# Kernel tuning notes

Measured on AMD Instinct MI355X. Metric: run time of the kernel, lower is better.

Reference implementation:

```python
import jax, jax.numpy as jnp
import numpy as np

N = 50000      # nodes
E = 800000     # edges (before self loops)
G = 64         # graphs in batch
IN = 128       # in_features
HID = 64       # hidden_dim per head
HEADS = 4
NC = 2         # num_classes
SLOPE = 0.2    # PyG GATConv negative_slope default


def setup_inputs() -> dict:
    key = jax.random.key(0)
    ks = jax.random.split(key, 16)
    s = 0.1
    HC = HID * HEADS
    inp = {
        "x": jax.random.normal(ks[0], (N, IN), jnp.float32),
        "edge_index": jax.random.randint(ks[1], (2, E), 0, N, jnp.int64),
        "batch": jnp.sort(jax.random.randint(ks[2], (N,), 0, G, jnp.int64)),
        # GATConv 1: lin weight [H*C, IN], att vecs [H, C], bias [H*C]
        "W1": jax.random.normal(ks[3], (HC, IN), jnp.float32) * s,
        "as1": jax.random.normal(ks[4], (HEADS, HID), jnp.float32) * s,
        "ad1": jax.random.normal(ks[5], (HEADS, HID), jnp.float32) * s,
        "b1": jnp.zeros((HC,), jnp.float32),
        # GATConv 2
        "W2": jax.random.normal(ks[6], (HC, HC), jnp.float32) * s,
        "as2": jax.random.normal(ks[7], (HEADS, HID), jnp.float32) * s,
        "ad2": jax.random.normal(ks[8], (HEADS, HID), jnp.float32) * s,
        "b2": jnp.zeros((HC,), jnp.float32),
        # GATConv 3
        "W3": jax.random.normal(ks[9], (HC, HC), jnp.float32) * s,
        "as3": jax.random.normal(ks[10], (HEADS, HID), jnp.float32) * s,
        "ad3": jax.random.normal(ks[11], (HEADS, HID), jnp.float32) * s,
        "b3": jnp.zeros((HC,), jnp.float32),
        # MLP head
        "fc1_w": jax.random.normal(ks[12], (HID, HC), jnp.float32) * s,
        "fc1_b": jnp.zeros((HID,), jnp.float32),
        "fc2_w": jax.random.normal(ks[13], (NC, HID), jnp.float32) * s,
        "fc2_b": jnp.zeros((NC,), jnp.float32),
    }
    return inp


def gat_conv(x, src, dst, W, a_src, a_dst, b):
    """PyG-style GATConv (concat=True, self loops already in src/dst)."""
    n = x.shape[0]
    h = (x @ W.T).reshape(n, HEADS, HID)            # [N,H,C]
    al_s = jnp.sum(h * a_src[None], axis=-1)        # [N,H]
    al_d = jnp.sum(h * a_dst[None], axis=-1)        # [N,H]
    e = jax.nn.leaky_relu(al_s[src] + al_d[dst], SLOPE)  # [Et,H]
    # segment softmax over edges grouped by destination node
    m = jax.ops.segment_max(e, dst, num_segments=n)      # [N,H]
    ex = jnp.exp(e - m[dst])
    den = jax.ops.segment_sum(ex, dst, num_segments=n)
    alpha = ex / (den[dst] + 1e-16)                      # [Et,H]
    out = jax.ops.segment_sum(h[src] * alpha[:, :, None], dst, num_segments=n)
    return out.reshape(n, HEADS * HID) + b


def reference(x, edge_index, batch, W1, as1, ad1, b1, W2, as2, ad2, b2,
              W3, as3, ad3, b3, fc1_w, fc1_b, fc2_w, fc2_b):
    loops = jnp.arange(N, dtype=edge_index.dtype)
    src = jnp.concatenate([edge_index[0], loops])   # add_self_loops=True
    dst = jnp.concatenate([edge_index[1], loops])

    h = jax.nn.relu(gat_conv(x, src, dst, W1, as1, ad1, b1))
    h = jax.nn.relu(gat_conv(h, src, dst, W2, as2, ad2, b2))
    h = gat_conv(h, src, dst, W3, as3, ad3, b3)

    # global_mean_pool over batch vector
    sums = jax.ops.segment_sum(h, batch, num_segments=G)          # [G,H*C]
    cnts = jax.ops.segment_sum(jnp.ones((N,), h.dtype), batch, num_segments=G)
    pooled = sums / jnp.maximum(cnts, 1.0)[:, None]

    z = jax.nn.relu(pooled @ fc1_w.T + fc1_b)
    return z @ fc2_w.T + fc2_b                                    # [G,NC]
```

## Files before the change

### kernel.cpp

```cpp
#include <hip/hip_runtime.h>
#include <hip/hip_bf16.h>

#define N_NODES 50000
#define E_EDGES 800000
#define ET (E_EDGES + N_NODES)
#define G_GRAPHS 64
#define IN_F 128
#define HID 64
#define HEADS 4
#define HC (HID * HEADS)
#define NC 2
#define SLOPE 0.2f
#define L2E 1.4426950408889634f

typedef float f32x4 __attribute__((ext_vector_type(4)));
typedef __bf16 bf16x8 __attribute__((ext_vector_type(8)));
typedef unsigned short us8 __attribute__((ext_vector_type(8)));
typedef unsigned short us4 __attribute__((ext_vector_type(4)));
typedef _Float16 h16x4 __attribute__((ext_vector_type(4)));

#define MFMA16(a, b, c) \
  __builtin_amdgcn_mfma_f32_16x16x32_bf16(__builtin_bit_cast(bf16x8, (a)), \
                                          __builtin_bit_cast(bf16x8, (b)), (c), 0, 0, 0)

__device__ inline unsigned short f2bf_rne(float f) {
  unsigned u = __builtin_bit_cast(unsigned, f);
  u += 0x7fffu + ((u >> 16) & 1u);
  return (unsigned short)(u >> 16);
}
__device__ inline float bf2f(unsigned short h) {
  unsigned u = ((unsigned)h) << 16;
  return __builtin_bit_cast(float, u);
}


__device__ inline void split4(const float* __restrict__ in, unsigned short* __restrict__ hi,
                              unsigned short* __restrict__ lo, int i) {
  float4 v = *(const float4*)&in[i];
  float f[4] = {v.x, v.y, v.z, v.w};
  us4 h, l;
#pragma unroll
  for (int j = 0; j < 4; j++) {
    unsigned short hb = f2bf_rne(f[j]);
    h[j] = hb;
    l[j] = f2bf_rne(f[j] - bf2f(hb));
  }
  *(us4*)&hi[i] = h;
  *(us4*)&lo[i] = l;
}

#define QX (N_NODES * IN_F / 4)
#define QW1 (HC * IN_F / 4)
#define QW2 (HC * HC / 4)
#define QTOT (QX + QW1 + 2 * QW2)

__global__ __launch_bounds__(256) void split_all_kernel(
    const float* __restrict__ x, const float* __restrict__ W1,
    const float* __restrict__ W2, const float* __restrict__ W3,
    unsigned short* __restrict__ xhi,
    unsigned short* __restrict__ w1h, unsigned short* __restrict__ w1l,
    unsigned short* __restrict__ w2h, unsigned short* __restrict__ w2l,
    unsigned short* __restrict__ w3h, unsigned short* __restrict__ w3l) {
  int q = blockIdx.x * 256 + threadIdx.x;
  if (q < QX) {
    int i = q * 4;
    float4 v = *(const float4*)&x[i];
    float f[4] = {v.x, v.y, v.z, v.w};
    us4 h;
#pragma unroll
    for (int j = 0; j < 4; j++) h[j] = f2bf_rne(f[j]);
    *(us4*)&xhi[i] = h;
  } else if (q < QX + QW1) {
    split4(W1, w1h, w1l, (q - QX) * 4);
  } else if (q < QX + QW1 + QW2) {
    split4(W2, w2h, w2l, (q - QX - QW1) * 4);
  } else {
    split4(W3, w3h, w3l, (q - QX - QW1 - QW2) * 4);
  }
}


__global__ void count_kernel(const int* __restrict__ ei, int* __restrict__ cnt) {
  int e = blockIdx.x * blockDim.x + threadIdx.x;
  if (e >= ET) return;
  int dst = (e < E_EDGES) ? ei[E_EDGES + e] : (e - E_EDGES);
  atomicAdd(&cnt[dst], 1);
}

#define SCAN_BLOCKS ((N_NODES + 255) / 256)

__global__ __launch_bounds__(256) void scan1_kernel(const int* __restrict__ cnt,
                                                    int* __restrict__ incl_buf,
                                                    int* __restrict__ partial) {
  __shared__ int ws[4];
  int tid = threadIdx.x, b = blockIdx.x;
  int wave = tid >> 6, lane = tid & 63;
  int i = b * 256 + tid;
  int v = (i < N_NODES) ? cnt[i] : 0;
  int x = v;
#pragma unroll
  for (int off = 1; off < 64; off <<= 1) {
    int t = __shfl_up(x, off, 64);
    if (lane >= off) x += t;
  }
  if (lane == 63) ws[wave] = x;
  __syncthreads();
  if (tid == 0) {
    int s = 0;
#pragma unroll
    for (int w = 0; w < 4; w++) { int t = ws[w]; ws[w] = s; s += t; }
    partial[b] = s;
  }
  __syncthreads();
  if (i < N_NODES) incl_buf[i] = x + ws[wave];
}

__global__ __launch_bounds__(256) void scan2_kernel(int* __restrict__ partial) {
  __shared__ int ws[4];
  int tid = threadIdx.x;
  int wave = tid >> 6, lane = tid & 63;
  int v = (tid < SCAN_BLOCKS) ? partial[tid] : 0;
  int x = v;
#pragma unroll
  for (int off = 1; off < 64; off <<= 1) {
    int t = __shfl_up(x, off, 64);
    if (lane >= off) x += t;
  }
  if (lane == 63) ws[wave] = x;
  __syncthreads();
  if (tid == 0) {
    int s = 0;
#pragma unroll
    for (int w = 0; w < 4; w++) { int t = ws[w]; ws[w] = s; s += t; }
  }
  __syncthreads();
  partial[tid] = x + ws[wave] - v;
}

__global__ __launch_bounds__(256) void scan3_kernel(const int* __restrict__ cnt,
                                                    int* __restrict__ incl_buf,
                                                    const int* __restrict__ partial,
                                                    int* __restrict__ rowptr,
                                                    int* __restrict__ cursor) {
  int tid = threadIdx.x, b = blockIdx.x;
  int i = b * 256 + tid;
  if (i >= N_NODES) return;
  int incl = incl_buf[i] + partial[b];
  rowptr[i + 1] = incl;
  cursor[i] = incl - cnt[i];
  if (i == 0) rowptr[0] = 0;
}

__global__ void scatter_kernel(const int* __restrict__ ei, int* __restrict__ cursor,
                               int* __restrict__ csr_src) {
  int e = blockIdx.x * blockDim.x + threadIdx.x;
  if (e >= ET) return;
  int src, dst;
  if (e < E_EDGES) { src = ei[e]; dst = ei[E_EDGES + e]; }
  else { src = e - E_EDGES; dst = src; }
  int pos = atomicAdd(&cursor[dst], 1);
  csr_src[pos] = src;
}


template <int K>
__global__ __launch_bounds__(256) void mfma_gemm_kernel(
    const unsigned short* __restrict__ A,
    const unsigned short* __restrict__ Whi, const unsigned short* __restrict__ Wlo,
    const float* __restrict__ a_s, const float* __restrict__ a_d,
    _Float16* __restrict__ hbuf16, float* __restrict__ als, float* __restrict__ ald) {
  __shared__ unsigned short As[4 * 64 * 8];
  __shared__ unsigned short Bs[2][4 * 256 * 8];

  int t = threadIdx.x;
  int mt = blockIdx.x;
  int w = t >> 6, lane = t & 63, lr = lane & 15, kg = lane >> 4;
  int srow = t >> 2, skg = t & 3;

  f32x4 acc[4][4];
#pragma unroll
  for (int m = 0; m < 4; m++)
#pragma unroll
    for (int nf = 0; nf < 4; nf++) {
      f32x4 z = {0.f, 0.f, 0.f, 0.f};
      acc[m][nf] = z;
    }

  int agrow = mt * 64 + srow;
  bool avalid = agrow < N_NODES;

  for (int k0 = 0; k0 < K; k0 += 32) {
    us8 va;
    if (avalid) {
      va = *(const us8*)&A[(size_t)agrow * K + k0 + skg * 8];
    } else {
      us8 z = {0, 0, 0, 0, 0, 0, 0, 0};
      va = z;
    }
    us8 vb0[4], vb1[4];
#pragma unroll
    for (int c = 0; c < 4; c++) {
      int n = srow + 64 * c;
      vb0[c] = *(const us8*)&Whi[(size_t)n * K + k0 + skg * 8];
      vb1[c] = *(const us8*)&Wlo[(size_t)n * K + k0 + skg * 8];
    }
    __syncthreads();
    *(us8*)&As[(skg * 64 + srow) * 8] = va;
#pragma unroll
    for (int c = 0; c < 4; c++) {
      int n = srow + 64 * c;
      *(us8*)&Bs[0][(skg * 256 + n) * 8] = vb0[c];
      *(us8*)&Bs[1][(skg * 256 + n) * 8] = vb1[c];
    }
    __syncthreads();

    us8 bh[4], bl[4];
#pragma unroll
    for (int nf = 0; nf < 4; nf++) {
      int n = w * 64 + nf * 16 + lr;
      bh[nf] = *(us8*)&Bs[0][(kg * 256 + n) * 8];
      bl[nf] = *(us8*)&Bs[1][(kg * 256 + n) * 8];
    }
#pragma unroll
    for (int m = 0; m < 4; m++) {
      int row = m * 16 + lr;
      us8 ah = *(us8*)&As[(kg * 64 + row) * 8];
#pragma unroll
      for (int nf = 0; nf < 4; nf++) {
        acc[m][nf] = MFMA16(ah, bh[nf], acc[m][nf]);
        acc[m][nf] = MFMA16(ah, bl[nf], acc[m][nf]);
      }
    }
  }

  int head = w;
  float asv[4], adv[4];
#pragma unroll
  for (int nf = 0; nf < 4; nf++) {
    asv[nf] = a_s[head * HID + nf * 16 + lr];
    adv[nf] = a_d[head * HID + nf * 16 + lr];
  }
#pragma unroll
  for (int m = 0; m < 4; m++) {
#pragma unroll
    for (int r = 0; r < 4; r++) {
      int grow = mt * 64 + m * 16 + kg * 4 + r;
      float ps = 0.f, pd = 0.f;
#pragma unroll
      for (int nf = 0; nf < 4; nf++) {
        float v = acc[m][nf][r];
        ps += v * asv[nf];
        pd += v * adv[nf];
        if (grow < N_NODES)
          hbuf16[(size_t)grow * HC + head * 64 + nf * 16 + lr] = (_Float16)v;
      }
#pragma unroll
      for (int msk = 1; msk < 16; msk <<= 1) {
        ps += __shfl_xor(ps, msk, 64);
        pd += __shfl_xor(pd, msk, 64);
      }
      if (lr == 0 && grow < N_NODES) {
        als[grow * HEADS + head] = ps * L2E;
        ald[grow * HEADS + head] = pd * L2E;
      }
    }
  }
}


template <int MODE>
__global__ __launch_bounds__(256) void agg_kernel(
    const _Float16* __restrict__ hbuf16, const float* __restrict__ alsE,
    const float* __restrict__ aldE, const int* __restrict__ rowptr,
    const int* __restrict__ csr_src, const float* __restrict__ bias,
    unsigned short* __restrict__ ohi, float* __restrict__ pooled,
    const int* __restrict__ batch) {
  int wave = threadIdx.x >> 6;
  int lane = threadIdx.x & 63;
  int v = blockIdx.x * 4 + wave;
  int head = lane >> 4;
  int lr = lane & 15;
  float myald = aldE[(unsigned)v * HEADS + head];
  int beg = rowptr[v];
  int n = rowptr[v + 1] - beg;

  float den = 0.f;
  f32x4 acc = {0.f, 0.f, 0.f, 0.f};
  const _Float16* hp = hbuf16 + (lane << 2);
  int bpbase = (lane & 48) << 2;

  for (int c = 0; c < n; c += 16) {
    int e = c + lr;
    int s = csr_src[beg + min(e, n - 1)];
    float a = alsE[(unsigned)s * HEADS + head] + myald;
    a = fmaxf(a, SLOPE * a);
    float ex = (e < n) ? __builtin_amdgcn_exp2f(a) : 0.f;
    den += ex;
    int rem = n - c;
    if (rem >= 16) {
#pragma unroll
      for (int j = 0; j < 16; j++) {
        int bp = bpbase + (j << 2);
        int sj = __builtin_amdgcn_ds_bpermute(bp, s);
        float exj = __builtin_bit_cast(
            float, __builtin_amdgcn_ds_bpermute(bp, __builtin_bit_cast(int, ex)));
        h16x4 hv = *(const h16x4*)(hp + ((unsigned)sj << 8));
        acc[0] += (float)hv[0] * exj;
        acc[1] += (float)hv[1] * exj;
        acc[2] += (float)hv[2] * exj;
        acc[3] += (float)hv[3] * exj;
      }
    } else {
      for (int j = 0; j < rem; j++) {
        int bp = bpbase + (j << 2);
        int sj = __builtin_amdgcn_ds_bpermute(bp, s);
        float exj = __builtin_bit_cast(
            float, __builtin_amdgcn_ds_bpermute(bp, __builtin_bit_cast(int, ex)));
        h16x4 hv = *(const h16x4*)(hp + ((unsigned)sj << 8));
        acc[0] += (float)hv[0] * exj;
        acc[1] += (float)hv[1] * exj;
        acc[2] += (float)hv[2] * exj;
        acc[3] += (float)hv[3] * exj;
      }
    }
  }
  den += __shfl_xor(den, 1, 64);
  den += __shfl_xor(den, 2, 64);
  den += __shfl_xor(den, 4, 64);
  den += __shfl_xor(den, 8, 64);

  float inv = 1.0f / (den + 1e-16f);
  float4 bv = *(const float4*)&bias[lane * 4];
  float o[4];
  o[0] = acc[0] * inv + bv.x;
  o[1] = acc[1] * inv + bv.y;
  o[2] = acc[2] * inv + bv.z;
  o[3] = acc[3] * inv + bv.w;

  if (MODE == 0) {
    us4 h;
#pragma unroll
    for (int j = 0; j < 4; j++) h[j] = f2bf_rne(fmaxf(o[j], 0.f));
    *(us4*)&ohi[(size_t)v * HC + lane * 4] = h;
  } else {
    __shared__ float pacc[4][HC];
    __shared__ int pg[4];
    f32x4 ov = {o[0], o[1], o[2], o[3]};
    *(f32x4*)&pacc[wave][lane * 4] = ov;
    if (lane == 0) pg[wave] = batch[v];
    __syncthreads();
    int c2 = threadIdx.x;
    int g0 = pg[0], g1 = pg[1], g2 = pg[2], g3 = pg[3];
    if (g0 == g1 && g1 == g2 && g2 == g3) {
      atomicAdd(&pooled[g0 * HC + c2], pacc[0][c2] + pacc[1][c2] + pacc[2][c2] + pacc[3][c2]);
    } else {
      atomicAdd(&pooled[g0 * HC + c2], pacc[0][c2]);
      atomicAdd(&pooled[g1 * HC + c2], pacc[1][c2]);
      atomicAdd(&pooled[g2 * HC + c2], pacc[2][c2]);
      atomicAdd(&pooled[g3 * HC + c2], pacc[3][c2]);
    }
  }
}


__global__ __launch_bounds__(64) void mlp_kernel(const float* __restrict__ pooled_sum,
                                                 const int* __restrict__ batch,
                                                 const float* __restrict__ w1,
                                                 const float* __restrict__ b1,
                                                 const float* __restrict__ w2,
                                                 const float* __restrict__ b2,
                                                 float* __restrict__ out) {
  int g = blockIdx.x;
  int j = threadIdx.x;
  int lo = 0, hi = N_NODES;
  while (lo < hi) { int mid = (lo + hi) >> 1; if (batch[mid] < g) lo = mid + 1; else hi = mid; }
  int start = lo;
  hi = N_NODES;
  while (lo < hi) { int mid = (lo + hi) >> 1; if (batch[mid] < g + 1) lo = mid + 1; else hi = mid; }
  float invc = 1.0f / fmaxf((float)(lo - start), 1.0f);
  __shared__ float z[HID];
  float acc = 0.f;
  for (int k = 0; k < HC; k++) acc += pooled_sum[g * HC + k] * w1[j * HC + k];
  z[j] = fmaxf(acc * invc + b1[j], 0.f);
  __syncthreads();
  if (j < NC) {
    float o = b2[j];
    for (int k = 0; k < HID; k++) o += z[k] * w2[j * HID + k];
    out[g * NC + j] = o;
  }
}


extern "C" void kernel_launch(void* const* d_in, const int* in_sizes, int n_in,
                              void* d_out, int out_size, void* d_ws, size_t ws_size,
                              hipStream_t stream) {
  const float* x    = (const float*)d_in[0];
  const int*   ei   = (const int*)d_in[1];
  const int*   batch= (const int*)d_in[2];
  const float* W1   = (const float*)d_in[3];
  const float* as1  = (const float*)d_in[4];
  const float* ad1  = (const float*)d_in[5];
  const float* b1   = (const float*)d_in[6];
  const float* W2   = (const float*)d_in[7];
  const float* as2  = (const float*)d_in[8];
  const float* ad2  = (const float*)d_in[9];
  const float* b2   = (const float*)d_in[10];
  const float* W3   = (const float*)d_in[11];
  const float* as3  = (const float*)d_in[12];
  const float* ad3  = (const float*)d_in[13];
  const float* b3   = (const float*)d_in[14];
  const float* fc1w = (const float*)d_in[15];
  const float* fc1b = (const float*)d_in[16];
  const float* fc2w = (const float*)d_in[17];
  const float* fc2b = (const float*)d_in[18];
  float* out = (float*)d_out;

  char* ws = (char*)d_ws;
  size_t off = 0;
  _Float16* hbuf16 = (_Float16*)(ws + off); off += (size_t)N_NODES * HC * 2;
  unsigned short* ahi = (unsigned short*)(ws + off); off += (size_t)N_NODES * HC * 2;
  unsigned short* xhi = (unsigned short*)(ws + off); off += (size_t)N_NODES * IN_F * 2;
  unsigned short* w1h = (unsigned short*)(ws + off); off += (size_t)HC * IN_F * 2;
  unsigned short* w1l = (unsigned short*)(ws + off); off += (size_t)HC * IN_F * 2;
  unsigned short* w2h = (unsigned short*)(ws + off); off += (size_t)HC * HC * 2;
  unsigned short* w2l = (unsigned short*)(ws + off); off += (size_t)HC * HC * 2;
  unsigned short* w3h = (unsigned short*)(ws + off); off += (size_t)HC * HC * 2;
  unsigned short* w3l = (unsigned short*)(ws + off); off += (size_t)HC * HC * 2;
  float* als    = (float*)(ws + off); off += (size_t)N_NODES * HEADS * 4;
  float* ald    = (float*)(ws + off); off += (size_t)N_NODES * HEADS * 4;
  float* pooled = (float*)(ws + off); off += (size_t)G_GRAPHS * HC * 4;
  int*   cnt    = (int*)(ws + off);   off += (size_t)N_NODES * 4;
  int*   cursor = (int*)(ws + off);   off += (size_t)N_NODES * 4;
  int*   csrsrc = (int*)(ws + off);   off += (size_t)ET * 4;
  int*   rowptr = (int*)(ws + off);   off += (size_t)(N_NODES + 1) * 4;
  int*   partial= (int*)(ws + off);   off += 256 * 4;

  split_all_kernel<<<(QTOT + 255) / 256, 256, 0, stream>>>(
      x, W1, W2, W3, xhi, w1h, w1l, w2h, w2l, w3h, w3l);

  hipMemsetAsync(cnt, 0, (size_t)N_NODES * 4, stream);
  hipMemsetAsync(pooled, 0, (size_t)G_GRAPHS * HC * 4, stream);
  count_kernel<<<(ET + 255) / 256, 256, 0, stream>>>(ei, cnt);
  scan1_kernel<<<SCAN_BLOCKS, 256, 0, stream>>>(cnt, cursor, partial);
  scan2_kernel<<<1, 256, 0, stream>>>(partial);
  scan3_kernel<<<SCAN_BLOCKS, 256, 0, stream>>>(cnt, cursor, partial, rowptr, cursor);
  scatter_kernel<<<(ET + 255) / 256, 256, 0, stream>>>(ei, cursor, csrsrc);

  dim3 gemm_grid((N_NODES + 63) / 64);
  int agg_grid = N_NODES / 4;

  mfma_gemm_kernel<IN_F><<<gemm_grid, 256, 0, stream>>>(xhi, w1h, w1l, as1, ad1, hbuf16, als, ald);
  agg_kernel<0><<<agg_grid, 256, 0, stream>>>(hbuf16, als, ald, rowptr, csrsrc, b1, ahi, nullptr, nullptr);
  mfma_gemm_kernel<HC><<<gemm_grid, 256, 0, stream>>>(ahi, w2h, w2l, as2, ad2, hbuf16, als, ald);
  agg_kernel<0><<<agg_grid, 256, 0, stream>>>(hbuf16, als, ald, rowptr, csrsrc, b2, ahi, nullptr, nullptr);
  mfma_gemm_kernel<HC><<<gemm_grid, 256, 0, stream>>>(ahi, w3h, w3l, as3, ad3, hbuf16, als, ald);
  agg_kernel<1><<<agg_grid, 256, 0, stream>>>(hbuf16, als, ald, rowptr, csrsrc, b3, nullptr, pooled, batch);

  mlp_kernel<<<G_GRAPHS, 64, 0, stream>>>(pooled, batch, fc1w, fc1b, fc2w, fc2b, out);
}
```

Measured before the change: 458.5 us.

## Store per-head hidden features head-major and aggregate one node per 16-lane group

The GEMM epilogue now writes hidden features in a head-major layout ([HEADS][N][HID]) instead of node-major rows. The aggregation kernel is restructured so each 16-lane group owns one destination node and loops over the four heads, walking edges one at a time with direct loads. This replaces the 16-edge chunking and ds_bpermute broadcasts, and each block now covers 16 nodes. The pooled reduction for the last layer is also reworked to run per head with run-length merging of graph ids. The cost is that edge indices and attention logits are re-read once per head. Lanes in a wave also diverge on node degree, and fewer independent gathers are in flight per wave.

```diff
diff --git a/kernel.cpp b/kernel.cpp
--- a/kernel.cpp
+++ b/kernel.cpp
@@ -234,6 +234,7 @@
   }
 
   int head = w;
+  _Float16* hout = hbuf16 + (size_t)head * ((size_t)N_NODES * HID);
   float asv[4], adv[4];
 #pragma unroll
   for (int nf = 0; nf < 4; nf++) {
@@ -252,7 +253,7 @@
         ps += v * asv[nf];
         pd += v * adv[nf];
         if (grow < N_NODES)
-          hbuf16[(size_t)grow * HC + head * 64 + nf * 16 + lr] = (_Float16)v;
+          hout[(size_t)grow * HID + nf * 16 + lr] = (_Float16)v;
       }
 #pragma unroll
       for (int msk = 1; msk < 16; msk <<= 1) {
@@ -275,89 +276,76 @@
     const int* __restrict__ csr_src, const float* __restrict__ bias,
     unsigned short* __restrict__ ohi, float* __restrict__ pooled,
     const int* __restrict__ batch) {
+  __shared__ float pacc[16][64];
+  __shared__ int pg[16];
   int wave = threadIdx.x >> 6;
   int lane = threadIdx.x & 63;
-  int v = blockIdx.x * 4 + wave;
-  int head = lane >> 4;
+  int grp = lane >> 4;
   int lr = lane & 15;
-  float myald = aldE[(unsigned)v * HEADS + head];
+  int nb = wave * 4 + grp;
+  int v = blockIdx.x * 16 + nb;
   int beg = rowptr[v];
   int n = rowptr[v + 1] - beg;
-
-  float den = 0.f;
-  f32x4 acc = {0.f, 0.f, 0.f, 0.f};
-  const _Float16* hp = hbuf16 + (lane << 2);
-  int bpbase = (lane & 48) << 2;
-
-  for (int c = 0; c < n; c += 16) {
-    int e = c + lr;
-    int s = csr_src[beg + min(e, n - 1)];
-    float a = alsE[(unsigned)s * HEADS + head] + myald;
-    a = fmaxf(a, SLOPE * a);
-    float ex = (e < n) ? __builtin_amdgcn_exp2f(a) : 0.f;
-    den += ex;
-    int rem = n - c;
-    if (rem >= 16) {
-#pragma unroll
-      for (int j = 0; j < 16; j++) {
-        int bp = bpbase + (j << 2);
-        int sj = __builtin_amdgcn_ds_bpermute(bp, s);
-        float exj = __builtin_bit_cast(
-            float, __builtin_amdgcn_ds_bpermute(bp, __builtin_bit_cast(int, ex)));
-        h16x4 hv = *(const h16x4*)(hp + ((unsigned)sj << 8));
-        acc[0] += (float)hv[0] * exj;
-        acc[1] += (float)hv[1] * exj;
-        acc[2] += (float)hv[2] * exj;
-        acc[3] += (float)hv[3] * exj;
+  const int* sp = csr_src + beg;
+  if (MODE == 1 && lane == 0) {
+    pg[wave * 4] = batch[v];
+    pg[wave * 4 + 1] = batch[v + 1];
+    pg[wave * 4 + 2] = batch[v + 2];
+    pg[wave * 4 + 3] = batch[v + 3];
+  }
+
+#pragma unroll
+  for (int p = 0; p < HEADS; p++) {
+    float aldv = aldE[(unsigned)v * HEADS + p];
+    float den = 0.f;
+    f32x4 acc = {0.f, 0.f, 0.f, 0.f};
+    const _Float16* hp = hbuf16 + (size_t)p * ((size_t)N_NODES * HID) + (lr << 2);
+#pragma unroll 2
+    for (int i = 0; i < n; i++) {
+      int s = sp[i];
+      float a = alsE[((unsigned)s << 2) + p] + aldv;
+      a = fmaxf(a, SLOPE * a);
+      float ex = __builtin_amdgcn_exp2f(a);
+      den += ex;
+      h16x4 hv = *(const h16x4*)(hp + ((unsigned)s << 6));
+      acc[0] += (float)hv[0] * ex;
+      acc[1] += (float)hv[1] * ex;
+      acc[2] += (float)hv[2] * ex;
+      acc[3] += (float)hv[3] * ex;
+    }
+    float inv = 1.0f / (den + 1e-16f);
+    float4 bv = *(const float4*)&bias[p * HID + lr * 4];
+    float o[4];
+    o[0] = acc[0] * inv + bv.x;
+    o[1] = acc[1] * inv + bv.y;
+    o[2] = acc[2] * inv + bv.z;
+    o[3] = acc[3] * inv + bv.w;
+
+    if (MODE == 0) {
+      us4 h;
+#pragma unroll
+      for (int j = 0; j < 4; j++) h[j] = f2bf_rne(fmaxf(o[j], 0.f));
+      *(us4*)&ohi[(size_t)v * HC + p * HID + lr * 4] = h;
+    } else {
+      f32x4 ov = {o[0], o[1], o[2], o[3]};
+      *(f32x4*)&pacc[nb][lr * 4] = ov;
+      __syncthreads();
+      int t = threadIdx.x;
+      if (t < 64) {
+        float s = pacc[0][t];
+        int gcur = pg[0];
+#pragma unroll
+        for (int k = 1; k < 16; k++) {
+          if (pg[k] != gcur) {
+            atomicAdd(&pooled[gcur * HC + p * HID + t], s);
+            s = 0.f;
+            gcur = pg[k];
+          }
+          s += pacc[k][t];
+        }
+        atomicAdd(&pooled[gcur * HC + p * HID + t], s);
       }
-    } else {
-      for (int j = 0; j < rem; j++) {
-        int bp = bpbase + (j << 2);
-        int sj = __builtin_amdgcn_ds_bpermute(bp, s);
-        float exj = __builtin_bit_cast(
-            float, __builtin_amdgcn_ds_bpermute(bp, __builtin_bit_cast(int, ex)));
-        h16x4 hv = *(const h16x4*)(hp + ((unsigned)sj << 8));
-        acc[0] += (float)hv[0] * exj;
-        acc[1] += (float)hv[1] * exj;
-        acc[2] += (float)hv[2] * exj;
-        acc[3] += (float)hv[3] * exj;
-      }
-    }
-  }
-  den += __shfl_xor(den, 1, 64);
-  den += __shfl_xor(den, 2, 64);
-  den += __shfl_xor(den, 4, 64);
-  den += __shfl_xor(den, 8, 64);
-
-  float inv = 1.0f / (den + 1e-16f);
-  float4 bv = *(const float4*)&bias[lane * 4];
-  float o[4];
-  o[0] = acc[0] * inv + bv.x;
-  o[1] = acc[1] * inv + bv.y;
-  o[2] = acc[2] * inv + bv.z;
-  o[3] = acc[3] * inv + bv.w;
-
-  if (MODE == 0) {
-    us4 h;
-#pragma unroll
-    for (int j = 0; j < 4; j++) h[j] = f2bf_rne(fmaxf(o[j], 0.f));
-    *(us4*)&ohi[(size_t)v * HC + lane * 4] = h;
-  } else {
-    __shared__ float pacc[4][HC];
-    __shared__ int pg[4];
-    f32x4 ov = {o[0], o[1], o[2], o[3]};
-    *(f32x4*)&pacc[wave][lane * 4] = ov;
-    if (lane == 0) pg[wave] = batch[v];
-    __syncthreads();
-    int c2 = threadIdx.x;
-    int g0 = pg[0], g1 = pg[1], g2 = pg[2], g3 = pg[3];
-    if (g0 == g1 && g1 == g2 && g2 == g3) {
-      atomicAdd(&pooled[g0 * HC + c2], pacc[0][c2] + pacc[1][c2] + pacc[2][c2] + pacc[3][c2]);
-    } else {
-      atomicAdd(&pooled[g0 * HC + c2], pacc[0][c2]);
-      atomicAdd(&pooled[g1 * HC + c2], pacc[1][c2]);
-      atomicAdd(&pooled[g2 * HC + c2], pacc[2][c2]);
-      atomicAdd(&pooled[g3 * HC + c2], pacc[3][c2]);
+      __syncthreads();
     }
   }
 }
@@ -447,7 +435,7 @@
   scatter_kernel<<<(ET + 255) / 256, 256, 0, stream>>>(ei, cursor, csrsrc);
 
   dim3 gemm_grid((N_NODES + 63) / 64);
-  int agg_grid = N_NODES / 4;
+  int agg_grid = N_NODES / 16;
 
   mfma_gemm_kernel<IN_F><<<gemm_grid, 256, 0, stream>>>(xhi, w1h, w1l, as1, ad1, hbuf16, als, ald);
   agg_kernel<0><<<agg_grid, 256, 0, stream>>>(hbuf16, als, ald, rowptr, csrsrc, b1, ahi, nullptr, nullptr);
```

New measurement: 502.5 us. 9.6% more time.
